# Optimization experiments

Hardware: AMD Instinct MI355X
Metric: run time of the kernel (lower is better)

The kernel has to match this reference:

```python
import jax, jax.numpy as jnp
import numpy as np

DIM = 2048
N_HEADS = 16
HEAD_DIM = DIM // N_HEADS  # 128
B, T = 2, 4096
K_CONV = 4
EPS = 1e-5


def _silu(x):
    return x * jax.nn.sigmoid(x)


def _l2norm(x):
    return x * jax.lax.rsqrt(jnp.sum(x * x, axis=-1, keepdims=True) + 1e-6)


def _short_conv(x, w):
    # depthwise causal conv1d, kernel K, then SiLU. x: [B,T,D], w: [D,K]
    K = w.shape[1]
    xp = jnp.pad(x, ((0, 0), (K - 1, 0), (0, 0)))
    y = xp[:, 0:x.shape[1], :] * w[:, 0]
    for i in range(1, K):
        y = y + xp[:, i:i + x.shape[1], :] * w[:, i]
    return _silu(y)


def _delta_rule(q, k, v, beta):
    # DeltaNet recurrence (math-equivalent to fla chunk_delta_rule with
    # use_qk_l2norm_in_kernel=True and default scale Dk**-0.5).
    # q,k: [B,T,H,Dk]; v: [B,T,H,Dv]; beta: [B,T,H]
    Dk = q.shape[-1]
    q = _l2norm(q) * (Dk ** -0.5)
    k = _l2norm(k)
    qT = jnp.swapaxes(q, 0, 1)  # [T,B,H,Dk]
    kT = jnp.swapaxes(k, 0, 1)
    vT = jnp.swapaxes(v, 0, 1)
    bT = jnp.swapaxes(beta, 0, 1)  # [T,B,H]

    def step(S, inp):
        qt, kt, vt, bt = inp
        # prediction error u = v - S^T k
        u = vt - jnp.einsum('bhk,bhkv->bhv', kt, S)
        S = S + bt[:, :, None, None] * kt[..., :, None] * u[..., None, :]
        o = jnp.einsum('bhk,bhkv->bhv', qt, S)
        return S, o

    S0 = jnp.zeros(q.shape[0:1] + q.shape[2:4] + (v.shape[-1],), dtype=q.dtype)
    _, o = jax.lax.scan(step, S0, (qT, kT, vT, bT))
    return jnp.swapaxes(o, 0, 1)  # [B,T,H,Dv]


def _rmsnorm(x, w):
    var = jnp.mean(x * x, axis=-1, keepdims=True)
    return x * jax.lax.rsqrt(var + EPS) * w


def setup_inputs() -> dict:
    key = jax.random.key(0)
    ks = jax.random.split(key, 16)
    std = 0.02
    inp = {
        'hidden_states': jax.random.normal(ks[0], (B, T, DIM), jnp.float32),
        'k_cache': jax.random.normal(ks[1], (B, T, N_HEADS, HEAD_DIM), jnp.float32),
        'v_cache': jax.random.normal(ks[2], (B, T, N_HEADS, HEAD_DIM), jnp.float32),
        'cos': jax.random.normal(ks[3], (B, T, HEAD_DIM), jnp.float32),
        'sin': jax.random.normal(ks[4], (B, T, HEAD_DIM), jnp.float32),
        'Wq': jax.random.normal(ks[5], (DIM, DIM), jnp.float32) * std,
        'Wk': jax.random.normal(ks[6], (DIM, DIM), jnp.float32) * std,
        'Wv': jax.random.normal(ks[7], (DIM, DIM), jnp.float32) * std,
        'Wo': jax.random.normal(ks[8], (DIM, DIM), jnp.float32) * std,
        'Wg': jax.random.normal(ks[9], (DIM, DIM), jnp.float32) * std,
        'Wb': jax.random.normal(ks[10], (DIM, N_HEADS), jnp.float32) * std,
        'conv_wq': jax.random.normal(ks[11], (DIM, K_CONV), jnp.float32) * 0.3,
        'conv_wk': jax.random.normal(ks[12], (DIM, K_CONV), jnp.float32) * 0.3,
        'conv_wv': jax.random.normal(ks[13], (DIM, K_CONV), jnp.float32) * 0.3,
        'norm_w': jnp.ones((HEAD_DIM,), jnp.float32),
    }
    return inp


def reference(hidden_states, k_cache, v_cache, cos, sin,
              Wq, Wk, Wv, Wo, Wg, Wb, conv_wq, conv_wk, conv_wv, norm_w):
    # Deterministic eval path of CrossSwitcher (mode='random', not training,
    # q_len>64): conv -> delta rule -> RMSNorm -> sigmoid gate -> o_proj.
    b, t, d = hidden_states.shape
    q = hidden_states @ Wq
    k = hidden_states @ Wk
    v = hidden_states @ Wv
    q = _short_conv(q, conv_wq)
    k = _short_conv(k, conv_wk)
    v = _short_conv(v, conv_wv)
    q = q.reshape(b, t, N_HEADS, HEAD_DIM)
    k = k.reshape(b, t, N_HEADS, HEAD_DIM)
    v = v.reshape(b, t, N_HEADS, HEAD_DIM)
    beta = jax.nn.sigmoid(hidden_states @ Wb)  # [B,T,H]
    o = _delta_rule(q, k, v, beta)             # [B,T,H,Dh]
    o = _rmsnorm(o, norm_w)
    g = (hidden_states @ Wg).reshape(b, t, N_HEADS, HEAD_DIM)
    o = o * jax.nn.sigmoid(g)
    o = o.reshape(b, t, d) @ Wo
    return o
```

## Files before the change

kernel.cpp:

```cpp
#include <hip/hip_runtime.h>
#include <cstdint>
#include <cstddef>

#define DEVI __device__ __forceinline__

typedef __attribute__((ext_vector_type(8))) short short8;
typedef __attribute__((ext_vector_type(4))) float floatx4;

constexpr int B_ = 2, T_ = 4096, D_ = 2048, H_ = 16, DH = 128;
constexpr int BT = B_ * T_;
constexpr int C_ = 64, NC = T_ / C_;

DEVI float bf2f(ushort u){ union { uint32_t i; float f; } v; v.i = ((uint32_t)u) << 16; return v.f; }
DEVI ushort f2bf(float f){ union { float f; uint32_t i; } v; v.f = f; uint32_t r = v.i + 0x7fff + ((v.i >> 16) & 1); return (ushort)(r >> 16); }
DEVI float sigm(float x){ return 1.f / (1.f + __expf(-x)); }

DEVI void async_load16(const void* g, void* l){
  __builtin_amdgcn_global_load_lds((const __attribute__((address_space(1))) unsigned int*)g,
                                   (__attribute__((address_space(3))) unsigned int*)l, 16, 0, 0);
}
DEVI floatx4 mfma16(short8 a, short8 b, floatx4 c){
  return __builtin_amdgcn_mfma_f32_16x16x32_bf16(a, b, c, 0, 0, 0);
}

__global__ __launch_bounds__(256) void cast_bf16_kernel(const float* __restrict__ x,
                                                        ushort* __restrict__ y, int n){
  int i = (blockIdx.x * 256 + threadIdx.x) * 8;
  if (i + 8 <= n){
    floatx4 a = *(const floatx4*)(x + i);
    floatx4 b = *(const floatx4*)(x + i + 4);
    short8 o;
    o[0]=(short)f2bf(a[0]); o[1]=(short)f2bf(a[1]); o[2]=(short)f2bf(a[2]); o[3]=(short)f2bf(a[3]);
    o[4]=(short)f2bf(b[0]); o[5]=(short)f2bf(b[1]); o[6]=(short)f2bf(b[2]); o[7]=(short)f2bf(b[3]);
    *(short8*)(y + i) = o;
  }
}

__global__ __launch_bounds__(256) void transpose_cast_kernel(const float* __restrict__ w,
                                                             ushort* __restrict__ wt){
  __shared__ float tile[32][33];
  int bx = blockIdx.x, by = blockIdx.y;
  int tx = threadIdx.x & 31, ty = threadIdx.x >> 5;
  #pragma unroll
  for (int j = 0; j < 4; ++j)
    tile[ty + j*8][tx] = w[(size_t)(by*32 + ty + j*8) * D_ + bx*32 + tx];
  __syncthreads();
  #pragma unroll
  for (int j = 0; j < 4; ++j){
    int n = bx*32 + ty + j*8, k = by*32 + tx;
    wt[(size_t)n * D_ + k] = f2bf(tile[tx][ty + j*8]);
  }
}

__global__ __launch_bounds__(256) void cast_wbT(const float* __restrict__ Wb,
                                                ushort* __restrict__ WbT){
  int c = blockIdx.x * 256 + threadIdx.x;
  #pragma unroll
  for (int h = 0; h < H_; ++h)
    WbT[h * D_ + c] = f2bf(Wb[(size_t)c * H_ + h]);
}

template<bool F32OUT>
__global__ __launch_bounds__(512) void gemm256k(const ushort* __restrict__ A,
                                                const ushort* __restrict__ Bt,
                                                void* __restrict__ Cv,
                                                int M, int N, int K){
  __shared__ __align__(16) ushort As[2][256 * 64];
  __shared__ __align__(16) ushort Bs[2][256 * 64];
  const int tid = threadIdx.x;
  const int w = tid >> 6, lane = tid & 63, l16 = lane & 15, lq = lane >> 4;
  const int wm = w >> 2, wn = w & 3;
  const int nbm = M >> 8;
  const int cpx = gridDim.x >> 3;
  const int wg = ((int)blockIdx.x & 7) * cpx + ((int)blockIdx.x >> 3);
  const int bm = wg % nbm, bn = wg / nbm;
  const int srow = tid >> 3;
  const int ce = ((tid & 7) ^ (srow & 7)) * 8;
  const ushort* Ab = A + (size_t)(bm*256 + srow) * K + ce;
  const ushort* Bb = Bt + (size_t)(bn*256 + srow) * K + ce;
  const int NT = K >> 6;

  floatx4 acc[8][4];
  #pragma unroll
  for (int i = 0; i < 8; ++i)
    #pragma unroll
    for (int j = 0; j < 4; ++j) acc[i][j] = (floatx4)0.f;

  auto stageA = [&](int kt, int buf){
    #pragma unroll
    for (int j = 0; j < 4; ++j)
      async_load16(Ab + (size_t)(j*64) * K + kt*64, (char*)&As[buf][0] + (j*512 + tid)*16);
  };
  auto stageB = [&](int kt, int buf){
    #pragma unroll
    for (int j = 0; j < 4; ++j)
      async_load16(Bb + (size_t)(j*64) * K + kt*64, (char*)&Bs[buf][0] + (j*512 + tid)*16);
  };
  auto frag = [&](const ushort* base, int row, int ks) -> short8 {
    int cB = (ks*64 + lq*16) ^ ((row & 7) << 4);
    return *(const short8*)(base + row*64 + (cB >> 1));
  };

  stageA(0, 0); stageB(0, 0);
  if (NT > 1){ stageA(1, 1); stageB(1, 1);
    asm volatile("s_waitcnt vmcnt(8)" ::: "memory");
  } else {
    asm volatile("s_waitcnt vmcnt(0)" ::: "memory");
  }
  __builtin_amdgcn_s_barrier();

  short8 afr[4][2], bfr[4][2];
  #pragma unroll 2
  for (int kt = 0; kt < NT; ++kt){
    const int buf = kt & 1;
    const ushort* pa = &As[buf][0];
    const ushort* pb = &Bs[buf][0];
    const bool st = (kt + 2 < NT);
    #pragma unroll
    for (int mf = 0; mf < 4; ++mf){
      afr[mf][0] = frag(pa, wm*128 + mf*16 + l16, 0);
      afr[mf][1] = frag(pa, wm*128 + mf*16 + l16, 1);
    }
    #pragma unroll
    for (int nf = 0; nf < 2; ++nf){
      bfr[nf][0] = frag(pb, wn*64 + nf*16 + l16, 0);
      bfr[nf][1] = frag(pb, wn*64 + nf*16 + l16, 1);
    }
    __builtin_amdgcn_sched_barrier(0);
    __builtin_amdgcn_s_barrier();
    asm volatile("s_waitcnt lgkmcnt(0)" ::: "memory");
    __builtin_amdgcn_sched_barrier(0);
    __builtin_amdgcn_s_setprio(1);
    #pragma unroll
    for (int mf = 0; mf < 4; ++mf)
      #pragma unroll
      for (int nf = 0; nf < 2; ++nf){
        acc[mf][nf] = mfma16(afr[mf][0], bfr[nf][0], acc[mf][nf]);
        acc[mf][nf] = mfma16(afr[mf][1], bfr[nf][1], acc[mf][nf]);
      }
    __builtin_amdgcn_s_setprio(0);
    __builtin_amdgcn_sched_barrier(0);
    __builtin_amdgcn_s_barrier();
    #pragma unroll
    for (int nf = 2; nf < 4; ++nf){
      bfr[nf][0] = frag(pb, wn*64 + nf*16 + l16, 0);
      bfr[nf][1] = frag(pb, wn*64 + nf*16 + l16, 1);
    }
    __builtin_amdgcn_sched_barrier(0);
    __builtin_amdgcn_s_barrier();
    asm volatile("s_waitcnt lgkmcnt(0)" ::: "memory");
    __builtin_amdgcn_sched_barrier(0);
    __builtin_amdgcn_s_setprio(1);
    #pragma unroll
    for (int mf = 0; mf < 4; ++mf)
      #pragma unroll
      for (int nf = 2; nf < 4; ++nf){
        acc[mf][nf] = mfma16(afr[mf][0], bfr[nf][0], acc[mf][nf]);
        acc[mf][nf] = mfma16(afr[mf][1], bfr[nf][1], acc[mf][nf]);
      }
    __builtin_amdgcn_s_setprio(0);
    __builtin_amdgcn_sched_barrier(0);
    __builtin_amdgcn_s_barrier();
    #pragma unroll
    for (int mf = 0; mf < 4; ++mf){
      afr[mf][0] = frag(pa, wm*128 + (mf + 4)*16 + l16, 0);
      afr[mf][1] = frag(pa, wm*128 + (mf + 4)*16 + l16, 1);
    }
    if (st) stageB(kt + 2, buf);
    __builtin_amdgcn_sched_barrier(0);
    __builtin_amdgcn_s_barrier();
    asm volatile("s_waitcnt lgkmcnt(0)" ::: "memory");
    __builtin_amdgcn_sched_barrier(0);
    __builtin_amdgcn_s_setprio(1);
    #pragma unroll
    for (int mf = 0; mf < 4; ++mf)
      #pragma unroll
      for (int nf = 2; nf < 4; ++nf){
        acc[mf + 4][nf] = mfma16(afr[mf][0], bfr[nf][0], acc[mf + 4][nf]);
        acc[mf + 4][nf] = mfma16(afr[mf][1], bfr[nf][1], acc[mf + 4][nf]);
      }
    __builtin_amdgcn_s_setprio(0);
    __builtin_amdgcn_sched_barrier(0);
    __builtin_amdgcn_s_barrier();
    if (st) stageA(kt + 2, buf);
    __builtin_amdgcn_sched_barrier(0);
    __builtin_amdgcn_s_barrier();
    __builtin_amdgcn_s_setprio(1);
    #pragma unroll
    for (int mf = 0; mf < 4; ++mf)
      #pragma unroll
      for (int nf = 0; nf < 2; ++nf){
        acc[mf + 4][nf] = mfma16(afr[mf][0], bfr[nf][0], acc[mf + 4][nf]);
        acc[mf + 4][nf] = mfma16(afr[mf][1], bfr[nf][1], acc[mf + 4][nf]);
      }
    __builtin_amdgcn_s_setprio(0);
    __builtin_amdgcn_sched_barrier(0);
    if (st)                   asm volatile("s_waitcnt vmcnt(8)" ::: "memory");
    else if (kt + 1 < NT)     asm volatile("s_waitcnt vmcnt(0)" ::: "memory");
    __builtin_amdgcn_s_barrier();
  }

  #pragma unroll
  for (int mf = 0; mf < 8; ++mf)
    #pragma unroll
    for (int nf = 0; nf < 4; ++nf)
      #pragma unroll
      for (int r = 0; r < 4; ++r){
        int row = bm*256 + wm*128 + mf*16 + lq*4 + r;
        int col = bn*256 + wn*64 + nf*16 + l16;
        if (F32OUT) ((float*)Cv)[(size_t)row * N + col] = acc[mf][nf][r];
        else        ((ushort*)Cv)[(size_t)row * N + col] = f2bf(acc[mf][nf][r]);
      }
}

__global__ __launch_bounds__(256) void conv3_kernel(
    const ushort* __restrict__ qpre, const ushort* __restrict__ kpre, const ushort* __restrict__ vpre,
    const float* __restrict__ cwq, const float* __restrict__ cwk, const float* __restrict__ cwv,
    ushort* __restrict__ qn, ushort* __restrict__ kn, ushort* __restrict__ vc){
  const int blk = blockIdx.x;
  const int b  = (blk * 8) >> 12;
  const int t0 = (blk * 8) & (T_ - 1);
  const int tid = threadIdx.x;
  const int ch0 = tid * 8;

  const ushort* srcs[3] = {qpre, kpre, vpre};
  const float*  cws[3]  = {cwq, cwk, cwv};
  ushort*       dsts[3] = {qn, kn, vc};

  #pragma unroll
  for (int s = 0; s < 3; ++s){
    floatx4 w[8];
    #pragma unroll
    for (int j = 0; j < 8; ++j) w[j] = *(const floatx4*)&cws[s][(ch0 + j) * 4];

    float xf[11][8];
    #pragma unroll
    for (int idx = 0; idx < 11; ++idx){
      int t = t0 - 3 + idx;
      short8 x = (t >= 0) ? *(const short8*)(srcs[s] + (size_t)(b*T_ + t)*D_ + ch0)
                          : (short8)(short)0;
      #pragma unroll
      for (int j = 0; j < 8; ++j) xf[idx][j] = bf2f((ushort)x[j]);
    }

    #pragma unroll
    for (int tt = 0; tt < 8; ++tt){
      float y[8];
      #pragma unroll
      for (int j = 0; j < 8; ++j){
        float a = xf[tt][j]*w[j][0] + xf[tt+1][j]*w[j][1]
                + xf[tt+2][j]*w[j][2] + xf[tt+3][j]*w[j][3];
        y[j] = a * sigm(a);
      }
      float scale = 1.f;
      if (s < 2){
        float ss = 0.f;
        #pragma unroll
        for (int j = 0; j < 8; ++j) ss += y[j]*y[j];
        #pragma unroll
        for (int m = 1; m < 16; m <<= 1) ss += __shfl_xor(ss, m);
        scale = rsqrtf(ss + 1e-6f);
        if (s == 0) scale *= 0.08838834764831845f;
      }
      short8 o;
      #pragma unroll
      for (int j = 0; j < 8; ++j) o[j] = (short)f2bf(y[j] * scale);
      *(short8*)(dsts[s] + (size_t)(b*T_ + t0 + tt)*D_ + ch0) = o;
    }
  }
}

__global__ __launch_bounds__(256) void beta_kernel(const ushort* __restrict__ hb,
                                                   const ushort* __restrict__ WbT,
                                                   float* __restrict__ beta){
  const int r = blockIdx.x * 4 + (threadIdx.x >> 6);
  const int lane = threadIdx.x & 63;
  float xf[32];
  #pragma unroll
  for (int i = 0; i < 4; ++i){
    short8 x = *(const short8*)(hb + (size_t)r * D_ + i*512 + lane*8);
    #pragma unroll
    for (int j = 0; j < 8; ++j) xf[i*8 + j] = bf2f((ushort)x[j]);
  }
  float res = 0.f;
  #pragma unroll
  for (int h = 0; h < H_; ++h){
    float s = 0.f;
    #pragma unroll
    for (int i = 0; i < 4; ++i){
      short8 wv = *(const short8*)(WbT + (size_t)h * D_ + i*512 + lane*8);
      #pragma unroll
      for (int j = 0; j < 8; ++j) s += xf[i*8 + j] * bf2f((ushort)wv[j]);
    }
    #pragma unroll
    for (int m = 1; m < 64; m <<= 1) s += __shfl_xor(s, m);
    if (lane == h) res = s;
  }
  if (lane < H_) beta[(size_t)r * H_ + lane] = sigm(res);
}

__global__ __launch_bounds__(256) void phase1(
    const ushort* __restrict__ kn, const ushort* __restrict__ vc, const float* __restrict__ beta,
    ushort* __restrict__ Wneg, ushort* __restrict__ U, ushort* __restrict__ KTg){
  __shared__ __align__(16) char smem[72960];
  ushort* Ks = (ushort*)smem;
  ushort* Xb = (ushort*)smem;
  ushort* KT = (ushort*)(smem + 17408);
  ushort* VT = (ushort*)(smem + 17408 + 18432);
  ushort* Xt = (ushort*)(smem + 17408 + 36864);
  ushort* Pb = (ushort*)(smem + 17408 + 36864 + 9216);
  float*  bet = (float*)(smem + 17408 + 36864 + 18432);

  const int bx = blockIdx.x;
  const int c = bx & 63, h = (bx >> 6) & 15, b = bx >> 10;
  const int t0 = c * 64;
  const int tid = threadIdx.x, w = tid >> 6, lane = tid & 63, l16 = lane & 15, lq = lane >> 4;

  {
    int i = tid >> 2, d0 = (tid & 3) * 32;
    const ushort* kp = kn + (size_t)(b*T_ + t0 + i) * D_ + h*DH + d0;
    const ushort* vp = vc + (size_t)(b*T_ + t0 + i) * D_ + h*DH + d0;
    #pragma unroll
    for (int j = 0; j < 4; ++j){
      short8 kv = *(const short8*)(kp + j*8);
      short8 vv = *(const short8*)(vp + j*8);
      *(short8*)&Ks[i*136 + d0 + j*8] = kv;
      #pragma unroll
      for (int e = 0; e < 8; ++e){
        int d = d0 + j*8 + e;
        KT[d*72 + i] = (ushort)kv[e];
        VT[d*72 + i] = (ushort)vv[e];
      }
    }
    if (tid < 64) bet[tid] = beta[(size_t)(b*T_ + t0 + tid) * H_ + h];
  }
  __syncthreads();

  floatx4 accL[4];
  #pragma unroll
  for (int fn = 0; fn < 4; ++fn) accL[fn] = (floatx4)0.f;
  #pragma unroll
  for (int ks = 0; ks < 4; ++ks){
    short8 a = *(const short8*)&Ks[(w*16 + l16)*136 + ks*32 + lq*8];
    #pragma unroll
    for (int fn = 0; fn < 4; ++fn){
      short8 bb = *(const short8*)&Ks[(fn*16 + l16)*136 + ks*32 + lq*8];
      accL[fn] = mfma16(a, bb, accL[fn]);
    }
  }
  __syncthreads();

  {
    size_t kb = (size_t)bx * (128 * 64);
    int d = tid >> 1, i0 = (tid & 1) * 32;
    #pragma unroll
    for (int j = 0; j < 4; ++j)
      *(short8*)(KTg + kb + d*64 + i0 + j*8) = *(const short8*)&KT[d*72 + i0 + j*8];
  }

  #pragma unroll
  for (int fn = 0; fn < 4; ++fn)
    #pragma unroll
    for (int r = 0; r < 4; ++r){
      int i = w*16 + lq*4 + r, j = fn*16 + l16;
      float v = (j < i) ? (-bet[i] * accL[fn][r]) : 0.f;
      ushort vb = f2bf(v);
      Xb[i*72 + j] = vb;
      Xt[j*72 + i] = vb;
      Pb[i*72 + j] = (i == j) ? f2bf(1.f) : vb;
    }
  __syncthreads();

  #pragma unroll 1
  for (int s = 0; s < 5; ++s){
    floatx4 accY[4];
    #pragma unroll
    for (int fn = 0; fn < 4; ++fn) accY[fn] = (floatx4)0.f;
    #pragma unroll
    for (int ks = 0; ks < 2; ++ks){
      short8 a = *(const short8*)&Xb[(w*16 + l16)*72 + ks*32 + lq*8];
      #pragma unroll
      for (int fn = 0; fn < 4; ++fn){
        short8 bb = *(const short8*)&Xt[(fn*16 + l16)*72 + ks*32 + lq*8];
        accY[fn] = mfma16(a, bb, accY[fn]);
      }
    }
    __syncthreads();
    #pragma unroll
    for (int fn = 0; fn < 4; ++fn)
      #pragma unroll
      for (int r = 0; r < 4; ++r){
        int i = w*16 + lq*4 + r, n = fn*16 + l16;
        ushort v = f2bf(accY[fn][r]);
        Xb[i*72 + n] = v;
        Xt[n*72 + i] = v;
      }
    __syncthreads();
    floatx4 accP[4];
    #pragma unroll
    for (int fn = 0; fn < 4; ++fn)
      #pragma unroll
      for (int r = 0; r < 4; ++r)
        accP[fn][r] = bf2f(Pb[(w*16 + lq*4 + r)*72 + fn*16 + l16]);
    #pragma unroll
    for (int ks = 0; ks < 2; ++ks){
      short8 a = *(const short8*)&Pb[(w*16 + l16)*72 + ks*32 + lq*8];
      #pragma unroll
      for (int fn = 0; fn < 4; ++fn){
        short8 bb = *(const short8*)&Xt[(fn*16 + l16)*72 + ks*32 + lq*8];
        accP[fn] = mfma16(a, bb, accP[fn]);
      }
    }
    #pragma unroll
    for (int fn = 0; fn < 4; ++fn)
      #pragma unroll
      for (int r = 0; r < 4; ++r)
        Pb[(w*16 + lq*4 + r)*72 + fn*16 + l16] = f2bf(accP[fn][r]);
    __syncthreads();
  }

  floatx4 accW[8], accU[8];
  #pragma unroll
  for (int fn = 0; fn < 8; ++fn){ accW[fn] = (floatx4)0.f; accU[fn] = (floatx4)0.f; }
  #pragma unroll
  for (int ks = 0; ks < 2; ++ks){
    short8 p = *(const short8*)&Pb[(w*16 + l16)*72 + ks*32 + lq*8];
    short8 a;
    #pragma unroll
    for (int e = 0; e < 8; ++e)
      a[e] = (short)f2bf(bf2f((ushort)p[e]) * bet[ks*32 + lq*8 + e]);
    #pragma unroll
    for (int fn = 0; fn < 8; ++fn){
      short8 bk = *(const short8*)&KT[(fn*16 + l16)*72 + ks*32 + lq*8];
      short8 bv = *(const short8*)&VT[(fn*16 + l16)*72 + ks*32 + lq*8];
      accW[fn] = mfma16(a, bk, accW[fn]);
      accU[fn] = mfma16(a, bv, accU[fn]);
    }
  }
  size_t base = (size_t)bx * (64 * 128);
  #pragma unroll
  for (int fn = 0; fn < 8; ++fn)
    #pragma unroll
    for (int r = 0; r < 4; ++r){
      int i = w*16 + lq*4 + r, d = fn*16 + l16;
      Wneg[base + i*128 + d] = f2bf(-accW[fn][r]);
      U[base + i*128 + d]    = f2bf(accU[fn][r]);
    }
}

__global__ __launch_bounds__(256) void phase2(
    const ushort* __restrict__ qn, const ushort* __restrict__ KTg,
    const ushort* __restrict__ Wneg, const ushort* __restrict__ U,
    ushort* __restrict__ UpT, ushort* __restrict__ Opart){
  __shared__ __align__(16) ushort Sb[32 * 136];
  __shared__ __align__(16) ushort Ws[64 * 136];
  __shared__ __align__(16) ushort Qs[64 * 136];
  __shared__ __align__(16) ushort KTc[128 * 72];
  __shared__ __align__(16) ushort Us[64 * 40];
  __shared__ __align__(16) ushort UT[32 * 72];

  const int bx = blockIdx.x;
  const int bh = bx >> 2, vs = bx & 3;
  const int b = bh >> 4, h = bh & 15;
  const int tid = threadIdx.x, w = tid >> 6, lane = tid & 63, l16 = lane & 15, lq = lane >> 4;

  for (int e = tid; e < 32*136; e += 256) Sb[e] = 0;

  floatx4 M[2][2];
  #pragma unroll
  for (int nf = 0; nf < 2; ++nf)
    #pragma unroll
    for (int kf = 0; kf < 2; ++kf) M[nf][kf] = (floatx4)0.f;

  const int si = tid >> 2, sd = (tid & 3) * 32;
  short8 rW[4], rQ[4], rK[4], rU;

  auto loadr = [&](int c){
    size_t cb = ((size_t)(bh*NC + c)) * (64 * 128);
    const ushort* wp = Wneg + cb + si*128 + sd;
    const ushort* qp = qn + ((size_t)(b*T_ + c*64 + si)) * D_ + h*DH + sd;
    const ushort* kp = KTg + cb + tid*32;
    #pragma unroll
    for (int j = 0; j < 4; ++j){
      rW[j] = *(const short8*)(wp + j*8);
      rQ[j] = *(const short8*)(qp + j*8);
      rK[j] = *(const short8*)(kp + j*8);
    }
    rU = *(const short8*)(U + cb + si*128 + vs*32 + (tid & 3)*8);
  };
  loadr(0);

  for (int c = 0; c < NC; ++c){
    #pragma unroll
    for (int j = 0; j < 4; ++j){
      *(short8*)&Ws[si*136 + sd + j*8] = rW[j];
      *(short8*)&Qs[si*136 + sd + j*8] = rQ[j];
      *(short8*)&KTc[(tid >> 1)*72 + (tid & 1)*32 + j*8] = rK[j];
    }
    *(short8*)&Us[si*40 + (tid & 3)*8] = rU;
    __syncthreads();
    if (c + 1 < NC) loadr(c + 1);

    floatx4 accU[2];
    #pragma unroll
    for (int fn = 0; fn < 2; ++fn)
      #pragma unroll
      for (int r = 0; r < 4; ++r)
        accU[fn][r] = bf2f(Us[(w*16 + lq*4 + r)*40 + fn*16 + l16]);
    #pragma unroll
    for (int ks = 0; ks < 4; ++ks){
      short8 a = *(const short8*)&Ws[(w*16 + l16)*136 + ks*32 + lq*8];
      #pragma unroll
      for (int fn = 0; fn < 2; ++fn){
        short8 bs = *(const short8*)&Sb[(fn*16 + l16)*136 + ks*32 + lq*8];
        accU[fn] = mfma16(a, bs, accU[fn]);
      }
    }
    #pragma unroll
    for (int fn = 0; fn < 2; ++fn)
      #pragma unroll
      for (int r = 0; r < 4; ++r)
        UT[(fn*16 + l16)*72 + w*16 + lq*4 + r] = f2bf(accU[fn][r]);
    __syncthreads();

    size_t cb = ((size_t)(bh*NC + c)) * (64 * 128);
    {
      int nl = tid >> 3, i0 = (tid & 7) * 8;
      *(short8*)(UpT + cb + (size_t)(vs*32 + nl)*64 + i0) = *(const short8*)&UT[nl*72 + i0];
    }
    floatx4 accO[2];
    #pragma unroll
    for (int fn = 0; fn < 2; ++fn) accO[fn] = (floatx4)0.f;
    #pragma unroll
    for (int ks = 0; ks < 4; ++ks){
      short8 a = *(const short8*)&Qs[(w*16 + l16)*136 + ks*32 + lq*8];
      #pragma unroll
      for (int fn = 0; fn < 2; ++fn){
        short8 bs = *(const short8*)&Sb[(fn*16 + l16)*136 + ks*32 + lq*8];
        accO[fn] = mfma16(a, bs, accO[fn]);
      }
    }
    #pragma unroll
    for (int fn = 0; fn < 2; ++fn)
      #pragma unroll
      for (int r = 0; r < 4; ++r){
        int i = w*16 + lq*4 + r;
        Opart[cb + (size_t)i*128 + vs*32 + fn*16 + l16] = f2bf(accO[fn][r]);
      }
    #pragma unroll
    for (int ks = 0; ks < 2; ++ks){
      short8 a0 = *(const short8*)&UT[(l16)*72 + ks*32 + lq*8];
      short8 a1 = *(const short8*)&UT[(16 + l16)*72 + ks*32 + lq*8];
      #pragma unroll
      for (int kf = 0; kf < 2; ++kf){
        short8 bk = *(const short8*)&KTc[(w*32 + kf*16 + l16)*72 + ks*32 + lq*8];
        M[0][kf] = mfma16(a0, bk, M[0][kf]);
        M[1][kf] = mfma16(a1, bk, M[1][kf]);
      }
    }
    __syncthreads();
    #pragma unroll
    for (int nf = 0; nf < 2; ++nf)
      #pragma unroll
      for (int kf = 0; kf < 2; ++kf)
        #pragma unroll
        for (int r = 0; r < 4; ++r)
          Sb[(nf*16 + lq*4 + r)*136 + w*32 + kf*16 + l16] = f2bf(M[nf][kf][r]);
  }
}

__global__ __launch_bounds__(256) void phase3(
    const ushort* __restrict__ qn, const ushort* __restrict__ kn,
    const ushort* __restrict__ UpT, const ushort* __restrict__ Opart,
    const ushort* g, const float* __restrict__ norm_w,
    ushort* og){
  __shared__ __align__(16) ushort Qs[64 * 136];
  __shared__ __align__(16) ushort Ks[64 * 136];
  __shared__ __align__(16) ushort UTs[128 * 72];
  __shared__ __align__(16) ushort Os[64 * 136];
  __shared__ __align__(16) ushort Gs[64 * 136];
  __shared__ __align__(16) ushort Ab[64 * 72];
  __shared__ float nw[128];

  const int bx = blockIdx.x;
  const int c = bx & 63, h = (bx >> 6) & 15, b = bx >> 10;
  const int t0 = c * 64;
  const int tid = threadIdx.x, w = tid >> 6, lane = tid & 63, l16 = lane & 15, lq = lane >> 4;
  const size_t cb = (size_t)bx * (64 * 128);

  {
    int i = tid >> 2, d0 = (tid & 3) * 32;
    const ushort* qp = qn + (size_t)(b*T_ + t0 + i) * D_ + h*DH + d0;
    const ushort* kp = kn + (size_t)(b*T_ + t0 + i) * D_ + h*DH + d0;
    const ushort* gp = g  + (size_t)(b*T_ + t0 + i) * D_ + h*DH + d0;
    const ushort* op = Opart + cb + i*128 + d0;
    #pragma unroll
    for (int j = 0; j < 4; ++j){
      *(short8*)&Qs[i*136 + d0 + j*8] = *(const short8*)(qp + j*8);
      *(short8*)&Ks[i*136 + d0 + j*8] = *(const short8*)(kp + j*8);
      *(short8*)&Gs[i*136 + d0 + j*8] = *(const short8*)(gp + j*8);
      *(short8*)&Os[i*136 + d0 + j*8] = *(const short8*)(op + j*8);
    }
    int n = tid >> 1, i0 = (tid & 1) * 32;
    #pragma unroll
    for (int j = 0; j < 4; ++j)
      *(short8*)&UTs[n*72 + i0 + j*8] = *(const short8*)(UpT + cb + n*64 + i0 + j*8);
    if (tid < 128) nw[tid] = norm_w[tid];
  }
  __syncthreads();

  floatx4 accA[4];
  #pragma unroll
  for (int fn = 0; fn < 4; ++fn) accA[fn] = (floatx4)0.f;
  #pragma unroll
  for (int ks = 0; ks < 4; ++ks){
    short8 a = *(const short8*)&Qs[(w*16 + l16)*136 + ks*32 + lq*8];
    #pragma unroll
    for (int fn = 0; fn < 4; ++fn){
      short8 bb = *(const short8*)&Ks[(fn*16 + l16)*136 + ks*32 + lq*8];
      accA[fn] = mfma16(a, bb, accA[fn]);
    }
  }
  #pragma unroll
  for (int fn = 0; fn < 4; ++fn)
    #pragma unroll
    for (int r = 0; r < 4; ++r){
      int i = w*16 + lq*4 + r, j = fn*16 + l16;
      Ab[i*72 + j] = f2bf((j <= i) ? accA[fn][r] : 0.f);
    }
  __syncthreads();

  floatx4 accO[8];
  #pragma unroll
  for (int fn = 0; fn < 8; ++fn)
    #pragma unroll
    for (int r = 0; r < 4; ++r)
      accO[fn][r] = bf2f(Os[(w*16 + lq*4 + r)*136 + fn*16 + l16]);
  #pragma unroll
  for (int ks = 0; ks < 2; ++ks){
    short8 a = *(const short8*)&Ab[(w*16 + l16)*72 + ks*32 + lq*8];
    #pragma unroll
    for (int fn = 0; fn < 8; ++fn){
      short8 bu = *(const short8*)&UTs[(fn*16 + l16)*72 + ks*32 + lq*8];
      accO[fn] = mfma16(a, bu, accO[fn]);
    }
  }
  #pragma unroll
  for (int r = 0; r < 4; ++r){
    float ss = 0.f;
    #pragma unroll
    for (int fn = 0; fn < 8; ++fn) ss += accO[fn][r] * accO[fn][r];
    #pragma unroll
    for (int m = 1; m < 16; m <<= 1) ss += __shfl_xor(ss, m);
    float rms = rsqrtf(ss * (1.f / 128.f) + 1e-5f);
    int i = w*16 + lq*4 + r;
    #pragma unroll
    for (int fn = 0; fn < 8; ++fn){
      int d = fn*16 + l16;
      float gv = bf2f(Gs[i*136 + d]);
      float o = accO[fn][r] * rms * nw[d] * sigm(gv);
      og[(size_t)(b*T_ + t0 + i) * D_ + h*DH + d] = f2bf(o);
    }
  }
}

extern "C" void kernel_launch(void* const* d_in, const int* in_sizes, int n_in,
                              void* d_out, int out_size, void* d_ws, size_t ws_size,
                              hipStream_t stream){
  const float* hidden = (const float*)d_in[0];
  const float* Wq = (const float*)d_in[5];
  const float* Wk = (const float*)d_in[6];
  const float* Wv = (const float*)d_in[7];
  const float* Wo = (const float*)d_in[8];
  const float* Wg = (const float*)d_in[9];
  const float* Wb = (const float*)d_in[10];
  const float* cwq = (const float*)d_in[11];
  const float* cwk = (const float*)d_in[12];
  const float* cwv = (const float*)d_in[13];
  const float* nw  = (const float*)d_in[14];

  char* ws = (char*)d_ws;
  size_t off = 0;
  auto alloc = [&](size_t bytes){ void* p = ws + off; off += (bytes + 255) & ~(size_t)255; return p; };
  const size_t SZ = (size_t)BT * D_ * 2;
  ushort* hb   = (ushort*)alloc(SZ);
  ushort* wqT  = (ushort*)alloc((size_t)D_*D_*2);
  ushort* wkT  = (ushort*)alloc((size_t)D_*D_*2);
  ushort* wvT  = (ushort*)alloc((size_t)D_*D_*2);
  ushort* wgT  = (ushort*)alloc((size_t)D_*D_*2);
  ushort* woT  = (ushort*)alloc((size_t)D_*D_*2);
  ushort* wbT  = (ushort*)alloc((size_t)H_*D_*2);
  ushort* qpre = (ushort*)alloc(SZ);
  ushort* kpre = (ushort*)alloc(SZ);
  ushort* vpre = (ushort*)alloc(SZ);
  ushort* kn   = (ushort*)alloc(SZ);
  ushort* vcv  = (ushort*)alloc(SZ);
  float*  beta = (float*)alloc((size_t)BT * H_ * 4);
  (void)in_sizes; (void)n_in; (void)out_size;
  if (off > ws_size) return;

  ushort* qn  = (ushort*)d_out;
  ushort* KTg = (ushort*)d_out + (size_t)BT * D_;

  cast_bf16_kernel<<<8192, 256, 0, stream>>>(hidden, hb, BT * D_);
  dim3 tg(64, 64);
  transpose_cast_kernel<<<tg, 256, 0, stream>>>(Wq, wqT);
  transpose_cast_kernel<<<tg, 256, 0, stream>>>(Wk, wkT);
  transpose_cast_kernel<<<tg, 256, 0, stream>>>(Wv, wvT);
  transpose_cast_kernel<<<tg, 256, 0, stream>>>(Wg, wgT);
  transpose_cast_kernel<<<tg, 256, 0, stream>>>(Wo, woT);
  cast_wbT<<<D_/256, 256, 0, stream>>>(Wb, wbT);

  const int NWG = (BT / 256) * (D_ / 256);
  gemm256k<false><<<NWG, 512, 0, stream>>>(hb, wqT, qpre, BT, D_, D_);
  gemm256k<false><<<NWG, 512, 0, stream>>>(hb, wkT, kpre, BT, D_, D_);
  gemm256k<false><<<NWG, 512, 0, stream>>>(hb, wvT, vpre, BT, D_, D_);

  conv3_kernel<<<BT/8, 256, 0, stream>>>(qpre, kpre, vpre, cwq, cwk, cwv, qn, kn, vcv);
  beta_kernel<<<BT/4, 256, 0, stream>>>(hb, wbT, beta);

  ushort* gpre = vpre;
  gemm256k<false><<<NWG, 512, 0, stream>>>(hb, wgT, gpre, BT, D_, D_);

  ushort* Wneg  = qpre;
  ushort* Ubuf  = kpre;
  ushort* Opart = hb;

  phase1<<<B_ * H_ * NC, 256, 0, stream>>>(kn, vcv, beta, Wneg, Ubuf, KTg);
  ushort* UpT = vcv;
  phase2<<<B_ * H_ * 4, 256, 0, stream>>>(qn, KTg, Wneg, Ubuf, UpT, Opart);
  ushort* og = gpre;
  phase3<<<B_ * H_ * NC, 256, 0, stream>>>(qn, kn, UpT, Opart, gpre, nw, og);

  gemm256k<true><<<NWG, 512, 0, stream>>>(og, woT, (float*)d_out, BT, D_, D_);
}
```

Measured before the change: 769.3 us.

## Fuse Q/K/V projections into one wide GEMM and remap phase2 blocks per XCD

Replaces three separate Q, K and V GEMM launches with one GEMM of width 3*D. It relies on the transposed wq/wk/wv buffers lying contiguously in the workspace and writes an interleaved [BT, 3D] output that the conv kernel reads with a 3D row stride. Buffers for gpre, Wneg and U are carved out of the fused region. phase2 block indices are remapped so the four v-slices of one (batch, head) land on the same XCD, meant to improve L2 sharing of the chunk data they all read. The fused GEMM depends on that implicit weight contiguity, which would break if the allocator layout changed.

```diff
diff --git a/kernel.cpp b/kernel.cpp
--- a/kernel.cpp
+++ b/kernel.cpp
@@ -10,6 +10,7 @@
 constexpr int B_ = 2, T_ = 4096, D_ = 2048, H_ = 16, DH = 128;
 constexpr int BT = B_ * T_;
 constexpr int C_ = 64, NC = T_ / C_;
+constexpr int RSQ = 3 * D_;
 
 DEVI float bf2f(ushort u){ union { uint32_t i; float f; } v; v.i = ((uint32_t)u) << 16; return v.f; }
 DEVI ushort f2bf(float f){ union { float f; uint32_t i; } v; v.f = f; uint32_t r = v.i + 0x7fff + ((v.i >> 16) & 1); return (ushort)(r >> 16); }
@@ -214,7 +215,7 @@
 }
 
 __global__ __launch_bounds__(256) void conv3_kernel(
-    const ushort* __restrict__ qpre, const ushort* __restrict__ kpre, const ushort* __restrict__ vpre,
+    const ushort* __restrict__ fqkv,
     const float* __restrict__ cwq, const float* __restrict__ cwk, const float* __restrict__ cwv,
     ushort* __restrict__ qn, ushort* __restrict__ kn, ushort* __restrict__ vc){
   const int blk = blockIdx.x;
@@ -223,12 +224,12 @@
   const int tid = threadIdx.x;
   const int ch0 = tid * 8;
 
-  const ushort* srcs[3] = {qpre, kpre, vpre};
   const float*  cws[3]  = {cwq, cwk, cwv};
   ushort*       dsts[3] = {qn, kn, vc};
 
   #pragma unroll
   for (int s = 0; s < 3; ++s){
+    const ushort* src = fqkv + s * D_;
     floatx4 w[8];
     #pragma unroll
     for (int j = 0; j < 8; ++j) w[j] = *(const floatx4*)&cws[s][(ch0 + j) * 4];
@@ -237,7 +238,7 @@
     #pragma unroll
     for (int idx = 0; idx < 11; ++idx){
       int t = t0 - 3 + idx;
-      short8 x = (t >= 0) ? *(const short8*)(srcs[s] + (size_t)(b*T_ + t)*D_ + ch0)
+      short8 x = (t >= 0) ? *(const short8*)(src + (size_t)(b*T_ + t)*RSQ + ch0)
                           : (short8)(short)0;
       #pragma unroll
       for (int j = 0; j < 8; ++j) xf[idx][j] = bf2f((ushort)x[j]);
@@ -460,7 +461,8 @@
   __shared__ __align__(16) ushort UT[32 * 72];
 
   const int bx = blockIdx.x;
-  const int bh = bx >> 2, vs = bx & 3;
+  const int xcd = bx & 7, j = bx >> 3;
+  const int bh = xcd * 4 + (j >> 2), vs = j & 3;
   const int b = bh >> 4, h = bh & 15;
   const int tid = threadIdx.x, w = tid >> 6, lane = tid & 63, l16 = lane & 15, lq = lane >> 4;
 
@@ -481,10 +483,10 @@
     const ushort* qp = qn + ((size_t)(b*T_ + c*64 + si)) * D_ + h*DH + sd;
     const ushort* kp = KTg + cb + tid*32;
     #pragma unroll
-    for (int j = 0; j < 4; ++j){
-      rW[j] = *(const short8*)(wp + j*8);
-      rQ[j] = *(const short8*)(qp + j*8);
-      rK[j] = *(const short8*)(kp + j*8);
+    for (int j2 = 0; j2 < 4; ++j2){
+      rW[j2] = *(const short8*)(wp + j2*8);
+      rQ[j2] = *(const short8*)(qp + j2*8);
+      rK[j2] = *(const short8*)(kp + j2*8);
     }
     rU = *(const short8*)(U + cb + si*128 + vs*32 + (tid & 3)*8);
   };
@@ -492,10 +494,10 @@
 
   for (int c = 0; c < NC; ++c){
     #pragma unroll
-    for (int j = 0; j < 4; ++j){
-      *(short8*)&Ws[si*136 + sd + j*8] = rW[j];
-      *(short8*)&Qs[si*136 + sd + j*8] = rQ[j];
-      *(short8*)&KTc[(tid >> 1)*72 + (tid & 1)*32 + j*8] = rK[j];
+    for (int j2 = 0; j2 < 4; ++j2){
+      *(short8*)&Ws[si*136 + sd + j2*8] = rW[j2];
+      *(short8*)&Qs[si*136 + sd + j2*8] = rQ[j2];
+      *(short8*)&KTc[(tid >> 1)*72 + (tid & 1)*32 + j2*8] = rK[j2];
     }
     *(short8*)&Us[si*40 + (tid & 3)*8] = rU;
     __syncthreads();
@@ -690,9 +692,7 @@
   ushort* wgT  = (ushort*)alloc((size_t)D_*D_*2);
   ushort* woT  = (ushort*)alloc((size_t)D_*D_*2);
   ushort* wbT  = (ushort*)alloc((size_t)H_*D_*2);
-  ushort* qpre = (ushort*)alloc(SZ);
-  ushort* kpre = (ushort*)alloc(SZ);
-  ushort* vpre = (ushort*)alloc(SZ);
+  ushort* fqkv = (ushort*)alloc(3*SZ);
   ushort* kn   = (ushort*)alloc(SZ);
   ushort* vcv  = (ushort*)alloc(SZ);
   float*  beta = (float*)alloc((size_t)BT * H_ * 4);
@@ -711,19 +711,22 @@
   transpose_cast_kernel<<<tg, 256, 0, stream>>>(Wo, woT);
   cast_wbT<<<D_/256, 256, 0, stream>>>(Wb, wbT);
 
-  const int NWG = (BT / 256) * (D_ / 256);
-  gemm256k<false><<<NWG, 512, 0, stream>>>(hb, wqT, qpre, BT, D_, D_);
-  gemm256k<false><<<NWG, 512, 0, stream>>>(hb, wkT, kpre, BT, D_, D_);
-  gemm256k<false><<<NWG, 512, 0, stream>>>(hb, wvT, vpre, BT, D_, D_);
-
-  conv3_kernel<<<BT/8, 256, 0, stream>>>(qpre, kpre, vpre, cwq, cwk, cwv, qn, kn, vcv);
+  {
+    const int NWG = (BT / 256) * (RSQ / 256);
+    gemm256k<false><<<NWG, 512, 0, stream>>>(hb, wqT, fqkv, BT, RSQ, D_);
+  }
+
+  conv3_kernel<<<BT/8, 256, 0, stream>>>(fqkv, cwq, cwk, cwv, qn, kn, vcv);
   beta_kernel<<<BT/4, 256, 0, stream>>>(hb, wbT, beta);
 
-  ushort* gpre = vpre;
-  gemm256k<false><<<NWG, 512, 0, stream>>>(hb, wgT, gpre, BT, D_, D_);
-
-  ushort* Wneg  = qpre;
-  ushort* Ubuf  = kpre;
+  ushort* gpre = fqkv;
+  ushort* Wneg = fqkv + (size_t)BT * D_;
+  ushort* Ubuf = fqkv + (size_t)2 * BT * D_;
+  {
+    const int NWG = (BT / 256) * (D_ / 256);
+    gemm256k<false><<<NWG, 512, 0, stream>>>(hb, wgT, gpre, BT, D_, D_);
+  }
+
   ushort* Opart = hb;
 
   phase1<<<B_ * H_ * NC, 256, 0, stream>>>(kn, vcv, beta, Wneg, Ubuf, KTg);
@@ -732,5 +735,8 @@
   ushort* og = gpre;
   phase3<<<B_ * H_ * NC, 256, 0, stream>>>(qn, kn, UpT, Opart, gpre, nw, og);
 
-  gemm256k<true><<<NWG, 512, 0, stream>>>(og, woT, (float*)d_out, BT, D_, D_);
-}
+  {
+    const int NWG = (BT / 256) * (D_ / 256);
+    gemm256k<true><<<NWG, 512, 0, stream>>>(og, woT, (float*)d_out, BT, D_, D_);
+  }
+}
```

Result: faster. 754.2 us (-2.0%).
